# Optimization experiments

Measured on AMD Instinct MI355X. Metric: run time of the kernel, lower is better.

Reference implementation:

```python
import jax, jax.numpy as jnp
import numpy as np

N = 50000
E = 800000
NEG_SLOPE = 0.2


def setup_inputs() -> dict:
    key = jax.random.key(0)
    ks = jax.random.split(key, 12)
    feat = jax.random.normal(ks[0], (N, 256), dtype=jnp.float32)
    src = jax.random.randint(ks[1], (E,), 0, N, dtype=jnp.int32)
    dst = jax.random.randint(ks[2], (E,), 0, N, dtype=jnp.int32)
    # layer 1: in=256 -> H=4, D=64 (concat 256)
    W1 = jax.random.normal(ks[3], (256, 256), dtype=jnp.float32) * (1.0 / np.sqrt(256))
    attn_l1 = jax.random.normal(ks[4], (4, 64), dtype=jnp.float32) * 0.1
    attn_r1 = jax.random.normal(ks[5], (4, 64), dtype=jnp.float32) * 0.1
    bias1 = jnp.zeros((256,), dtype=jnp.float32)
    # layer 2: in=256 -> H=1, D=128
    W2 = jax.random.normal(ks[6], (256, 128), dtype=jnp.float32) * (1.0 / np.sqrt(256))
    attn_l2 = jax.random.normal(ks[7], (1, 128), dtype=jnp.float32) * 0.1
    attn_r2 = jax.random.normal(ks[8], (1, 128), dtype=jnp.float32) * 0.1
    bias2 = jnp.zeros((128,), dtype=jnp.float32)
    return {"feat": feat, "src": src, "dst": dst,
            "W1": W1, "attn_l1": attn_l1, "attn_r1": attn_r1, "bias1": bias1,
            "W2": W2, "attn_l2": attn_l2, "attn_r2": attn_r2, "bias2": bias2}


def gat_conv(feat, src, dst, W, attn_l, attn_r, bias, apply_relu):
    H, D = attn_l.shape
    n = feat.shape[0]
    ft = (feat @ W).reshape(n, H, D)                      # [N,H,D]
    el = jnp.einsum('nhd,hd->nh', ft, attn_l)             # [N,H]
    er = jnp.einsum('nhd,hd->nh', ft, attn_r)             # [N,H]
    e = el[src] + er[dst]                                 # [E,H]  u_add_v
    e = jnp.where(e > 0, e, NEG_SLOPE * e)                # leaky_relu
    # edge softmax grouped by dst
    m = jax.ops.segment_max(e, dst, num_segments=n)       # [N,H]
    ex = jnp.exp(e - m[dst])
    denom = jax.ops.segment_sum(ex, dst, num_segments=n)  # [N,H]
    a = ex / denom[dst]                                   # [E,H]
    msg = ft[src] * a[:, :, None]                         # [E,H,D]
    out = jax.ops.segment_sum(msg, dst, num_segments=n)   # [N,H,D]
    out = out + bias.reshape(1, H, D)
    out = out.reshape(n, H * D)                           # concat_out
    if apply_relu:
        out = jax.nn.relu(out)
    return out


def reference(feat, src, dst, W1, attn_l1, attn_r1, bias1, W2, attn_l2, attn_r2, bias2):
    h = gat_conv(feat, src, dst, W1, attn_l1, attn_r1, bias1, apply_relu=True)
    h = gat_conv(h, src, dst, W2, attn_l2, attn_r2, bias2, apply_relu=False)
    return h
```

## Files before the change

### kernel.cpp

```cpp
#include <hip/hip_runtime.h>

#define NEG_SLOPE 0.2f

typedef short s16x8 __attribute__((ext_vector_type(8)));
typedef float f32x4 __attribute__((ext_vector_type(4)));

__device__ __forceinline__ unsigned short f2bf(float f) {
    unsigned int u = __float_as_uint(f);
    unsigned int r = (u + 0x7fffu + ((u >> 16) & 1u)) >> 16;
    return (unsigned short)r;
}
__device__ __forceinline__ float bf2f(unsigned int us) {
    return __uint_as_float(us << 16);
}


__global__ void fill_k(const int* __restrict__ src, const int* __restrict__ dst,
                       int* __restrict__ cnt, int* __restrict__ ovf_n,
                       int* __restrict__ bucket,
                       int* __restrict__ ovf_dst, int* __restrict__ ovf_src, int E,
                       const float* __restrict__ W1, const float* __restrict__ al1,
                       const float* __restrict__ ar1,
                       const float* __restrict__ W2, const float* __restrict__ al2,
                       const float* __restrict__ ar2,
                       float* __restrict__ wl1, float* __restrict__ wl2,
                       unsigned short* __restrict__ Bt1h, unsigned short* __restrict__ Bt1l,
                       unsigned short* __restrict__ Bt2h, unsigned short* __restrict__ Bt2l) {
    const int b = blockIdx.x;
    if (b == 0) {
        int k = threadIdx.x;
        #pragma unroll
        for (int h = 0; h < 4; h++) {
            float sl = 0.f, sr = 0.f;
            #pragma unroll 8
            for (int d = 0; d < 64; d++) {
                float wv = W1[k * 256 + h * 64 + d];
                sl = fmaf(wv, al1[h * 64 + d], sl);
                sr = fmaf(wv, ar1[h * 64 + d], sr);
            }
            wl1[k * 8 + h] = sl;
            wl1[k * 8 + 4 + h] = sr;
        }
        float sl = 0.f, sr = 0.f;
        #pragma unroll 8
        for (int d = 0; d < 128; d++) {
            float wv = W2[k * 128 + d];
            sl = fmaf(wv, al2[d], sl);
            sr = fmaf(wv, ar2[d], sr);
        }
        wl2[k * 2 + 0] = sl;
        wl2[k * 2 + 1] = sr;
        return;
    }
    if (b <= 4) {
        int c = (b - 1) * 64 + (threadIdx.x >> 2);
        int kq = threadIdx.x & 3;
        #pragma unroll 8
        for (int kk = 0; kk < 64; kk++) {
            int k = kq + kk * 4;
            float w = W1[k * 256 + c];
            unsigned short h = f2bf(w);
            unsigned short l = f2bf(w - bf2f(h));
            Bt1h[c * 256 + k] = h;
            Bt1l[c * 256 + k] = l;
        }
        return;
    }
    if (b <= 6) {
        int c = (b - 5) * 64 + (threadIdx.x >> 2);
        int kq = threadIdx.x & 3;
        #pragma unroll 8
        for (int kk = 0; kk < 64; kk++) {
            int k = kq + kk * 4;
            float w = W2[k * 128 + c];
            unsigned short h = f2bf(w);
            unsigned short l = f2bf(w - bf2f(h));
            Bt2h[c * 256 + k] = h;
            Bt2l[c * 256 + k] = l;
        }
        return;
    }
    int e = (b - 7) * 256 + threadIdx.x;
    if (e < E) {
        int d = dst[e];
        int pos = atomicAdd(&cnt[d], 1);
        if (pos < 64) {
            bucket[(d << 6) + pos] = src[e];
        } else {
            int j = atomicAdd(ovf_n, 1);
            ovf_dst[j] = d;
            ovf_src[j] = src[e];
        }
    }
}


__global__ __launch_bounds__(256) void prep_k(const float* __restrict__ feat,
                                              const float* __restrict__ wl1,
                                              unsigned short* __restrict__ Ah,
                                              unsigned short* __restrict__ Al,
                                              float* __restrict__ el1,
                                              float* __restrict__ er1, int Nn) {
    const int lane = threadIdx.x & 63, wid = threadIdx.x >> 6;
    const int n = blockIdx.x * 4 + wid;
    if (n >= Nn) return;
    float4 f = ((const float4*)(feat + (size_t)n * 256))[lane];
    unsigned short h0 = f2bf(f.x), h1 = f2bf(f.y), h2 = f2bf(f.z), h3 = f2bf(f.w);
    unsigned short l0 = f2bf(f.x - bf2f(h0)), l1 = f2bf(f.y - bf2f(h1));
    unsigned short l2 = f2bf(f.z - bf2f(h2)), l3 = f2bf(f.w - bf2f(h3));
    uint2 hv, lv;
    hv.x = (unsigned)h0 | ((unsigned)h1 << 16);
    hv.y = (unsigned)h2 | ((unsigned)h3 << 16);
    lv.x = (unsigned)l0 | ((unsigned)l1 << 16);
    lv.y = (unsigned)l2 | ((unsigned)l3 << 16);
    ((uint2*)(Ah + (size_t)n * 256))[lane] = hv;
    ((uint2*)(Al + (size_t)n * 256))[lane] = lv;

    float ff[4] = {f.x, f.y, f.z, f.w};
    float pa[4] = {0.f, 0.f, 0.f, 0.f}, pb[4] = {0.f, 0.f, 0.f, 0.f};
    const float* wp = wl1 + lane * 32;
    #pragma unroll
    for (int j = 0; j < 4; j++) {
        float4 wa = *(const float4*)(wp + j * 8);
        float4 wb = *(const float4*)(wp + j * 8 + 4);
        pa[0] = fmaf(ff[j], wa.x, pa[0]); pa[1] = fmaf(ff[j], wa.y, pa[1]);
        pa[2] = fmaf(ff[j], wa.z, pa[2]); pa[3] = fmaf(ff[j], wa.w, pa[3]);
        pb[0] = fmaf(ff[j], wb.x, pb[0]); pb[1] = fmaf(ff[j], wb.y, pb[1]);
        pb[2] = fmaf(ff[j], wb.z, pb[2]); pb[3] = fmaf(ff[j], wb.w, pb[3]);
    }
    #pragma unroll
    for (int h = 0; h < 4; h++) {
        #pragma unroll
        for (int o = 32; o > 0; o >>= 1) {
            pa[h] += __shfl_xor(pa[h], o);
            pb[h] += __shfl_xor(pb[h], o);
        }
    }
    if (lane == 0) {
        ((float4*)el1)[n] = float4{pa[0], pa[1], pa[2], pa[3]};
        ((float4*)er1)[n] = float4{pb[0], pb[1], pb[2], pb[3]};
    }
}


__global__ __launch_bounds__(256) void gemm_k(const unsigned short* __restrict__ Ah,
                                              const unsigned short* __restrict__ Al,
                                              const unsigned short* __restrict__ Bh,
                                              const unsigned short* __restrict__ Bl,
                                              unsigned short* __restrict__ Cb,
                                              int M, int Nc) {
    __shared__ __align__(16) unsigned short As_h[128][56], As_l[128][56];
    __shared__ __align__(16) unsigned short Bs_h[64][56], Bs_l[64][56];

    const int tid = threadIdx.x;
    const int lane = tid & 63, wid = tid >> 6;
    const int row0 = blockIdx.y * 128;
    const int col0 = blockIdx.x * 64;
    const int wm = (wid & 1) * 64;
    const int wn = (wid >> 1) * 32;
    const int quad = lane >> 4, mrow = lane & 15;

    const int a_row = tid >> 1;
    const int a_k = (tid & 1) * 16;
    const int b_col = tid >> 2;
    const int b_k = (tid & 3) * 8;

    const size_t a_off = (size_t)min(row0 + a_row, M - 1) * 256 + a_k;
    const size_t b_off = (size_t)(col0 + b_col) * 256 + b_k;

    f32x4 acc[4][2];
    #pragma unroll
    for (int i = 0; i < 4; i++)
        #pragma unroll
        for (int j = 0; j < 2; j++) acc[i][j] = f32x4{0.f, 0.f, 0.f, 0.f};

    uint4 rah0 = *(const uint4*)(Ah + a_off);
    uint4 rah1 = *(const uint4*)(Ah + a_off + 8);
    uint4 ral0 = *(const uint4*)(Al + a_off);
    uint4 ral1 = *(const uint4*)(Al + a_off + 8);
    uint4 rbh  = *(const uint4*)(Bh + b_off);
    uint4 rbl  = *(const uint4*)(Bl + b_off);

    for (int kt = 0; kt < 8; kt++) {
        __syncthreads();
        *(uint4*)&As_h[a_row][a_k]     = rah0;
        *(uint4*)&As_h[a_row][a_k + 8] = rah1;
        *(uint4*)&As_l[a_row][a_k]     = ral0;
        *(uint4*)&As_l[a_row][a_k + 8] = ral1;
        *(uint4*)&Bs_h[b_col][b_k] = rbh;
        *(uint4*)&Bs_l[b_col][b_k] = rbl;
        __syncthreads();
        if (kt < 7) {
            size_t ao = a_off + (size_t)(kt + 1) * 32;
            size_t bo = b_off + (size_t)(kt + 1) * 32;
            rah0 = *(const uint4*)(Ah + ao);
            rah1 = *(const uint4*)(Ah + ao + 8);
            ral0 = *(const uint4*)(Al + ao);
            ral1 = *(const uint4*)(Al + ao + 8);
            rbh  = *(const uint4*)(Bh + bo);
            rbl  = *(const uint4*)(Bl + bo);
        }
        s16x8 ah[4], al4[4], bh[2], bl[2];
        #pragma unroll
        for (int i = 0; i < 4; i++) {
            ah[i]  = *(const s16x8*)&As_h[wm + 16 * i + mrow][quad * 8];
            al4[i] = *(const s16x8*)&As_l[wm + 16 * i + mrow][quad * 8];
        }
        #pragma unroll
        for (int j = 0; j < 2; j++) {
            bh[j] = *(const s16x8*)&Bs_h[wn + 16 * j + mrow][quad * 8];
            bl[j] = *(const s16x8*)&Bs_l[wn + 16 * j + mrow][quad * 8];
        }
        #pragma unroll
        for (int i = 0; i < 4; i++)
            #pragma unroll
            for (int j = 0; j < 2; j++) {
                acc[i][j] = __builtin_amdgcn_mfma_f32_16x16x32_bf16(ah[i],  bh[j], acc[i][j], 0, 0, 0);
                acc[i][j] = __builtin_amdgcn_mfma_f32_16x16x32_bf16(ah[i],  bl[j], acc[i][j], 0, 0, 0);
                acc[i][j] = __builtin_amdgcn_mfma_f32_16x16x32_bf16(al4[i], bh[j], acc[i][j], 0, 0, 0);
            }
    }

    #pragma unroll
    for (int i = 0; i < 4; i++) {
        #pragma unroll
        for (int j = 0; j < 2; j++) {
            int col = col0 + wn + 16 * j + mrow;
            int rbase = row0 + wm + 16 * i + quad * 4;
            #pragma unroll
            for (int r = 0; r < 4; r++) {
                int row = rbase + r;
                if (row < M) Cb[(size_t)row * Nc + col] = f2bf(acc[i][j][r]);
            }
        }
    }
}


__device__ __forceinline__ void fma8(float* acc, float wgt, uint4 u) {
    acc[0] = fmaf(wgt, bf2f(u.x & 0xffff), acc[0]);
    acc[1] = fmaf(wgt, bf2f(u.x >> 16),    acc[1]);
    acc[2] = fmaf(wgt, bf2f(u.y & 0xffff), acc[2]);
    acc[3] = fmaf(wgt, bf2f(u.y >> 16),    acc[3]);
    acc[4] = fmaf(wgt, bf2f(u.z & 0xffff), acc[4]);
    acc[5] = fmaf(wgt, bf2f(u.z >> 16),    acc[5]);
    acc[6] = fmaf(wgt, bf2f(u.w & 0xffff), acc[6]);
    acc[7] = fmaf(wgt, bf2f(u.w >> 16),    acc[7]);
}

template <int H, int D, bool RELU, bool FUSE2>
__global__ __launch_bounds__(256) void fagg_k(const unsigned short* __restrict__ ft,
                                              const float* __restrict__ el,
                                              const float* __restrict__ er,
                                              const int* __restrict__ cnt,
                                              const int* __restrict__ bucket,
                                              const int* __restrict__ ovf_n,
                                              const int* __restrict__ ovf_dst,
                                              const int* __restrict__ ovf_src,
                                              const float* __restrict__ bias,
                                              float* __restrict__ out, int n_nodes,
                                              unsigned short* __restrict__ oh,
                                              unsigned short* __restrict__ ol,
                                              const float* __restrict__ wl2,
                                              float* __restrict__ el2,
                                              float* __restrict__ er2) {
    constexpr int HD = H * D;
    constexpr int LPE = HD / 8;
    constexpr int EPI = 64 / LPE;
    constexpr int SH = (HD == 256) ? 9 : 8;
    const int lane = threadIdx.x & 63;
    const int w = threadIdx.x >> 6;
    const int n = blockIdx.x * 4 + w;
    __shared__ int   s_src[4][64];
    __shared__ float s_a[4][64 * H];
    if (n >= n_nodes) return;
    const int deg = cnt[n];
    const int lane_sub = lane & (LPE - 1);
    const int q = lane / LPE;
    const int c0 = lane_sub * 8;
    const int h_of = c0 / D;
    const unsigned lsub16 = (unsigned)(lane_sub * 16);
    const char* fb = (const char*)ft;
    const char* eb = (const char*)el;

    float ern[H];
    #pragma unroll
    for (int h = 0; h < H; h++) ern[h] = er[n * H + h];

    float acc[8];
    #pragma unroll
    for (int t = 0; t < 8; t++) acc[t] = 0.f;

    const int* s_src_w = s_src[w];
    const float* s_a_w = s_a[w];

    if (deg <= 64) {
        const bool act = lane < deg;
        int sv = act ? bucket[(n << 6) + lane] : 0;
        s_src[w][lane] = sv;
        float evr[H];
        if constexpr (H == 4) {
            float4 e4 = *(const float4*)(eb + ((unsigned)sv << 4));
            evr[0] = e4.x; evr[1] = e4.y; evr[2] = e4.z; evr[3] = e4.w;
        } else {
            evr[0] = *(const float*)(eb + ((unsigned)sv << 2));
        }
        const int rc = (deg + EPI - 1) & ~(EPI - 1);
        const int nl = rc / EPI;
        const int nl0 = nl < 16 ? nl : 16;
        uint4 vv[8];
        #pragma unroll
        for (int i = 0; i < 8; i++) {
            if (i < nl0) {
                unsigned bo = ((unsigned)s_src_w[i * EPI + q] << SH) + lsub16;
                vv[i] = *(const uint4*)(fb + bo);
            }
        }
        float ex[H], sm[H];
        #pragma unroll
        for (int h = 0; h < H; h++) {
            float t = evr[h] + ern[h];
            t = t > 0.f ? t : NEG_SLOPE * t;
            ex[h] = act ? __expf(t) : 0.f;
            sm[h] = ex[h];
        }
        #pragma unroll
        for (int h = 0; h < H; h++)
            for (int o = 32; o > 0; o >>= 1) sm[h] += __shfl_xor(sm[h], o);
        #pragma unroll
        for (int h = 0; h < H; h++)
            s_a[w][lane * H + h] = ex[h] * (sm[h] > 0.f ? 1.f / sm[h] : 0.f);
        #pragma unroll
        for (int i = 0; i < 16; i++) {
            if (i < nl0) {
                float wt = s_a_w[(i * EPI + q) * H + h_of];
                fma8(acc, wt, vv[i & 7]);
                if (i + 8 < nl0) {
                    unsigned bo = ((unsigned)s_src_w[(i + 8) * EPI + q] << SH) + lsub16;
                    vv[i & 7] = *(const uint4*)(fb + bo);
                }
            }
        }
        for (int e = 16 * EPI + q; e < rc; e += EPI) {
            unsigned bo = ((unsigned)s_src_w[e] << SH) + lsub16;
            uint4 v = *(const uint4*)(fb + bo);
            fma8(acc, s_a_w[e * H + h_of], v);
        }
    } else {
        const int novf = *ovf_n;
        int sv0 = bucket[(n << 6) + lane];
        s_src[w][lane] = sv0;
        float sm[H];
        #pragma unroll
        for (int h = 0; h < H; h++) sm[h] = 0.f;
        {
            float evr[H];
            if constexpr (H == 4) {
                float4 e4 = ((const float4*)el)[sv0];
                evr[0] = e4.x; evr[1] = e4.y; evr[2] = e4.z; evr[3] = e4.w;
            } else evr[0] = el[sv0];
            #pragma unroll
            for (int h = 0; h < H; h++) {
                float t = evr[h] + ern[h];
                t = t > 0.f ? t : NEG_SLOPE * t;
                sm[h] += __expf(t);
            }
        }
        for (int i = lane; i < novf; i += 64) {
            if (ovf_dst[i] == n) {
                int sv = ovf_src[i];
                float evr[H];
                if constexpr (H == 4) {
                    float4 e4 = ((const float4*)el)[sv];
                    evr[0] = e4.x; evr[1] = e4.y; evr[2] = e4.z; evr[3] = e4.w;
                } else evr[0] = el[sv];
                #pragma unroll
                for (int h = 0; h < H; h++) {
                    float t = evr[h] + ern[h];
                    t = t > 0.f ? t : NEG_SLOPE * t;
                    sm[h] += __expf(t);
                }
            }
        }
        #pragma unroll
        for (int h = 0; h < H; h++)
            for (int o = 32; o > 0; o >>= 1) sm[h] += __shfl_xor(sm[h], o);
        float inv[H];
        #pragma unroll
        for (int h = 0; h < H; h++) inv[h] = (sm[h] > 0.f) ? (1.f / sm[h]) : 0.f;
        {
            float evr[H];
            if constexpr (H == 4) {
                float4 e4 = ((const float4*)el)[sv0];
                evr[0] = e4.x; evr[1] = e4.y; evr[2] = e4.z; evr[3] = e4.w;
            } else evr[0] = el[sv0];
            #pragma unroll
            for (int h = 0; h < H; h++) {
                float t = evr[h] + ern[h];
                t = t > 0.f ? t : NEG_SLOPE * t;
                s_a[w][lane * H + h] = __expf(t) * inv[h];
            }
        }
        for (int e = q; e < 64; e += EPI) {
            unsigned bo = ((unsigned)s_src_w[e] << SH) + lsub16;
            uint4 v = *(const uint4*)(fb + bo);
            fma8(acc, s_a_w[e * H + h_of], v);
        }
        for (int i = 0; i < novf; i++) {
            if (ovf_dst[i] != n) continue;
            int sv = ovf_src[i];
            float elh, ernh, invh;
            if constexpr (H == 4) {
                float4 e4 = ((const float4*)el)[sv];
                elh  = (h_of & 2) ? ((h_of & 1) ? e4.w : e4.z)
                                  : ((h_of & 1) ? e4.y : e4.x);
                ernh = (h_of & 2) ? ((h_of & 1) ? ern[3] : ern[2])
                                  : ((h_of & 1) ? ern[1] : ern[0]);
                invh = (h_of & 2) ? ((h_of & 1) ? inv[3] : inv[2])
                                  : ((h_of & 1) ? inv[1] : inv[0]);
            } else {
                elh = el[sv]; ernh = ern[0]; invh = inv[0];
            }
            float t = elh + ernh;
            t = t > 0.f ? t : NEG_SLOPE * t;
            float wt = __expf(t) * invh;
            uint4 v = *(const uint4*)(fb + (((unsigned)sv << SH) + lsub16));
            if (q == 0) fma8(acc, wt, v);
        }
    }

    #pragma unroll
    for (int t = 0; t < 8; t++) {
        #pragma unroll
        for (int s = LPE; s < 64; s <<= 1) acc[t] += __shfl_xor(acc[t], s);
    }
    if (lane < LPE) {
        float4 b0 = ((const float4*)bias)[lane * 2];
        float4 b1 = ((const float4*)bias)[lane * 2 + 1];
        float v[8] = {acc[0] + b0.x, acc[1] + b0.y, acc[2] + b0.z, acc[3] + b0.w,
                      acc[4] + b1.x, acc[5] + b1.y, acc[6] + b1.z, acc[7] + b1.w};
        if (RELU) {
            #pragma unroll
            for (int t = 0; t < 8; t++) v[t] = fmaxf(v[t], 0.f);
        }
        if constexpr (FUSE2) {
            unsigned short hh[8], ll[8];
            #pragma unroll
            for (int t = 0; t < 8; t++) {
                hh[t] = f2bf(v[t]);
                ll[t] = f2bf(v[t] - bf2f(hh[t]));
            }
            uint4 hv, lv;
            hv.x = (unsigned)hh[0] | ((unsigned)hh[1] << 16);
            hv.y = (unsigned)hh[2] | ((unsigned)hh[3] << 16);
            hv.z = (unsigned)hh[4] | ((unsigned)hh[5] << 16);
            hv.w = (unsigned)hh[6] | ((unsigned)hh[7] << 16);
            lv.x = (unsigned)ll[0] | ((unsigned)ll[1] << 16);
            lv.y = (unsigned)ll[2] | ((unsigned)ll[3] << 16);
            lv.z = (unsigned)ll[4] | ((unsigned)ll[5] << 16);
            lv.w = (unsigned)ll[6] | ((unsigned)ll[7] << 16);
            ((uint4*)(oh + (size_t)n * HD))[lane] = hv;
            ((uint4*)(ol + (size_t)n * HD))[lane] = lv;
            float pa = 0.f, pb = 0.f;
            #pragma unroll
            for (int t = 0; t < 8; t++) {
                float2 wv = ((const float2*)wl2)[lane * 8 + t];
                pa = fmaf(v[t], wv.x, pa);
                pb = fmaf(v[t], wv.y, pb);
            }
            #pragma unroll
            for (int o = 16; o > 0; o >>= 1) {
                pa += __shfl_xor(pa, o);
                pb += __shfl_xor(pb, o);
            }
            if (lane == 0) { el2[n] = pa; er2[n] = pb; }
        } else {
            float4 o0{v[0], v[1], v[2], v[3]};
            float4 o1{v[4], v[5], v[6], v[7]};
            float4* op = (float4*)out + (size_t)n * (HD / 4) + lane * 2;
            op[0] = o0;
            op[1] = o1;
        }
    }
}


extern "C" void kernel_launch(void* const* d_in, const int* in_sizes, int n_in,
                              void* d_out, int out_size, void* d_ws, size_t ws_size,
                              hipStream_t stream) {
    const float* feat    = (const float*)d_in[0];
    const int*   src     = (const int*)d_in[1];
    const int*   dst     = (const int*)d_in[2];
    const float* W1      = (const float*)d_in[3];
    const float* attn_l1 = (const float*)d_in[4];
    const float* attn_r1 = (const float*)d_in[5];
    const float* bias1   = (const float*)d_in[6];
    const float* W2      = (const float*)d_in[7];
    const float* attn_l2 = (const float*)d_in[8];
    const float* attn_r2 = (const float*)d_in[9];
    const float* bias2   = (const float*)d_in[10];
    float* out = (float*)d_out;

    const int N = in_sizes[0] / 256;
    const int E = in_sizes[1];
    const int nbE = (E + 255) / 256;

    char* ws = (char*)d_ws;
    size_t o = 0;
    auto alloc = [&](size_t bytes) -> void* {
        void* p = ws + o;
        o = (o + bytes + 255) & ~(size_t)255;
        return p;
    };
    int* cnt     = (int*)alloc((size_t)(N + 64) * 4);
    int* ovf_n   = cnt + N;
    int* bucket  = (int*)alloc((size_t)N * 64 * 4);
    int* ovf_dst = (int*)alloc((size_t)E * 4);
    int* ovf_src = (int*)alloc((size_t)E * 4);
    float* wl1 = (float*)alloc(256 * 8 * 4);
    float* wl2 = (float*)alloc(256 * 2 * 4);
    float* el1 = (float*)alloc((size_t)N * 4 * 4);
    float* er1 = (float*)alloc((size_t)N * 4 * 4);
    float* el2 = (float*)alloc((size_t)N * 4);
    float* er2 = (float*)alloc((size_t)N * 4);
    unsigned short* ft1b = (unsigned short*)alloc((size_t)N * 256 * 2);
    unsigned short* Ah   = (unsigned short*)alloc((size_t)N * 256 * 2);
    unsigned short* Al   = (unsigned short*)alloc((size_t)N * 256 * 2);
    unsigned short* Bt1h = (unsigned short*)alloc((size_t)256 * 256 * 2);
    unsigned short* Bt1l = (unsigned short*)alloc((size_t)256 * 256 * 2);
    unsigned short* Bt2h = (unsigned short*)alloc((size_t)128 * 256 * 2);
    unsigned short* Bt2l = (unsigned short*)alloc((size_t)128 * 256 * 2);
    unsigned short* ft2b = ft1b;
    unsigned short* h1h  = Ah;
    unsigned short* h1l  = Al;

    hipMemsetAsync(cnt, 0, (size_t)(N + 64) * 4, stream);
    fill_k<<<7 + nbE, 256, 0, stream>>>(src, dst, cnt, ovf_n, bucket, ovf_dst, ovf_src, E,
                                        W1, attn_l1, attn_r1, W2, attn_l2, attn_r2,
                                        wl1, wl2, Bt1h, Bt1l, Bt2h, Bt2l);
    prep_k<<<(N + 3) / 4, 256, 0, stream>>>(feat, wl1, Ah, Al, el1, er1, N);

    gemm_k<<<dim3(4, (N + 127) / 128), 256, 0, stream>>>(Ah, Al, Bt1h, Bt1l, ft1b, N, 256);
    fagg_k<4, 64, true, true><<<(N + 3) / 4, 256, 0, stream>>>(ft1b, el1, er1, cnt, bucket,
                                                               ovf_n, ovf_dst, ovf_src,
                                                               bias1, nullptr, N,
                                                               h1h, h1l, wl2, el2, er2);

    gemm_k<<<dim3(2, (N + 127) / 128), 256, 0, stream>>>(h1h, h1l, Bt2h, Bt2l, ft2b, N, 128);
    fagg_k<1, 128, false, false><<<(N + 3) / 4, 256, 0, stream>>>(ft2b, el2, er2, cnt, bucket,
                                                                  ovf_n, ovf_dst, ovf_src,
                                                                  bias2, out, N,
                                                                  nullptr, nullptr, nullptr,
                                                                  nullptr, nullptr);
}
```

Before: 374.5 us.

## Two-pass binned edge partition to replace global atomic bucket fill

Edge bucketing now happens in two passes. First, edges are partitioned into 256-node destination bins using LDS-local counting and one global atomic per bin per block, with (src,dst) pairs written into scratch that reuses the ft1b buffer. Second, one block per bin fills each node's bucket using LDS atomics, merged with the feature prep kernel. This removes the per-edge global atomics on node counters at the cost of an extra pass over the pair data. Correctness now depends on the global overflow count, so any overflow sends every node in aggregation down the slow path.

```diff
diff --git a/kernel.cpp b/kernel.cpp
--- a/kernel.cpp
+++ b/kernel.cpp
@@ -1,6 +1,7 @@
 #include <hip/hip_runtime.h>
 
 #define NEG_SLOPE 0.2f
+#define BIN_CAP 8192
 
 typedef short s16x8 __attribute__((ext_vector_type(8)));
 typedef float f32x4 __attribute__((ext_vector_type(4)));
@@ -15,17 +16,18 @@
 }
 
 
-__global__ void fill_k(const int* __restrict__ src, const int* __restrict__ dst,
-                       int* __restrict__ cnt, int* __restrict__ ovf_n,
-                       int* __restrict__ bucket,
-                       int* __restrict__ ovf_dst, int* __restrict__ ovf_src, int E,
-                       const float* __restrict__ W1, const float* __restrict__ al1,
-                       const float* __restrict__ ar1,
-                       const float* __restrict__ W2, const float* __restrict__ al2,
-                       const float* __restrict__ ar2,
-                       float* __restrict__ wl1, float* __restrict__ wl2,
-                       unsigned short* __restrict__ Bt1h, unsigned short* __restrict__ Bt1l,
-                       unsigned short* __restrict__ Bt2h, unsigned short* __restrict__ Bt2l) {
+__global__ __launch_bounds__(256) void binpart_k(
+        const int* __restrict__ src, const int* __restrict__ dst, int E,
+        int* __restrict__ bin_cur, int* __restrict__ ovf_n,
+        int2* __restrict__ pairs,
+        int* __restrict__ ovf_dst, int* __restrict__ ovf_src,
+        const float* __restrict__ W1, const float* __restrict__ al1,
+        const float* __restrict__ ar1,
+        const float* __restrict__ W2, const float* __restrict__ al2,
+        const float* __restrict__ ar2,
+        float* __restrict__ wl1, float* __restrict__ wl2,
+        unsigned short* __restrict__ Bt1h, unsigned short* __restrict__ Bt1l,
+        unsigned short* __restrict__ Bt2h, unsigned short* __restrict__ Bt2l) {
     const int b = blockIdx.x;
     if (b == 0) {
         int k = threadIdx.x;
@@ -80,29 +82,92 @@
         }
         return;
     }
-    int e = (b - 7) * 256 + threadIdx.x;
-    if (e < E) {
-        int d = dst[e];
-        int pos = atomicAdd(&cnt[d], 1);
-        if (pos < 64) {
-            bucket[(d << 6) + pos] = src[e];
-        } else {
-            int j = atomicAdd(ovf_n, 1);
-            ovf_dst[j] = d;
-            ovf_src[j] = src[e];
-        }
-    }
-}
-
-
-__global__ __launch_bounds__(256) void prep_k(const float* __restrict__ feat,
-                                              const float* __restrict__ wl1,
-                                              unsigned short* __restrict__ Ah,
-                                              unsigned short* __restrict__ Al,
-                                              float* __restrict__ el1,
-                                              float* __restrict__ er1, int Nn) {
+    __shared__ int l_cnt[256];
+    __shared__ int l_base[256];
+    const int tid = threadIdx.x;
+    const int base_e = (b - 7) * 2048 + tid * 8;
+    int s[8], d[8], bn[8], rk[8];
+    bool v[8];
+    if (base_e + 7 < E) {
+        int4 a0 = *(const int4*)(src + base_e);
+        int4 a1 = *(const int4*)(src + base_e + 4);
+        int4 c0 = *(const int4*)(dst + base_e);
+        int4 c1 = *(const int4*)(dst + base_e + 4);
+        s[0]=a0.x; s[1]=a0.y; s[2]=a0.z; s[3]=a0.w;
+        s[4]=a1.x; s[5]=a1.y; s[6]=a1.z; s[7]=a1.w;
+        d[0]=c0.x; d[1]=c0.y; d[2]=c0.z; d[3]=c0.w;
+        d[4]=c1.x; d[5]=c1.y; d[6]=c1.z; d[7]=c1.w;
+        #pragma unroll
+        for (int i = 0; i < 8; i++) v[i] = true;
+    } else {
+        #pragma unroll
+        for (int i = 0; i < 8; i++) {
+            int e = base_e + i;
+            v[i] = e < E;
+            s[i] = v[i] ? src[e] : 0;
+            d[i] = v[i] ? dst[e] : 0;
+        }
+    }
+    l_cnt[tid] = 0;
+    __syncthreads();
+    #pragma unroll
+    for (int i = 0; i < 8; i++) {
+        bn[i] = d[i] >> 8;
+        if (v[i]) rk[i] = atomicAdd(&l_cnt[bn[i]], 1);
+    }
+    __syncthreads();
+    {
+        int c = l_cnt[tid];
+        if (c > 0) l_base[tid] = atomicAdd(&bin_cur[tid * 16], c);
+    }
+    __syncthreads();
+    #pragma unroll
+    for (int i = 0; i < 8; i++) {
+        if (v[i]) {
+            int pos = l_base[bn[i]] + rk[i];
+            if (pos < BIN_CAP) {
+                int2 p; p.x = s[i]; p.y = d[i];
+                pairs[(size_t)bn[i] * BIN_CAP + pos] = p;
+            } else {
+                int j = atomicAdd(ovf_n, 1);
+                ovf_dst[j] = d[i]; ovf_src[j] = s[i];
+            }
+        }
+    }
+}
+
+
+__global__ __launch_bounds__(256) void prepfill_k(
+        const int* __restrict__ bin_cur, const int2* __restrict__ pairs,
+        int* __restrict__ cnt, int* __restrict__ bucket,
+        int* __restrict__ ovf_n, int* __restrict__ ovf_dst, int* __restrict__ ovf_src,
+        const float* __restrict__ feat, const float* __restrict__ wl1,
+        unsigned short* __restrict__ Ah, unsigned short* __restrict__ Al,
+        float* __restrict__ el1, float* __restrict__ er1, int Nn, int nbin) {
+    if ((int)blockIdx.x < nbin) {
+        __shared__ int l_cnt[256];
+        const int b = blockIdx.x;
+        const int tid = threadIdx.x;
+        l_cnt[tid] = 0;
+        __syncthreads();
+        const int ec = min(bin_cur[b * 16], BIN_CAP);
+        const int2* pp = pairs + (size_t)b * BIN_CAP;
+        for (int i = tid; i < ec; i += 256) {
+            int2 p = pp[i];
+            int pos = atomicAdd(&l_cnt[p.y & 255], 1);
+            if (pos < 64) bucket[((size_t)p.y << 6) + pos] = p.x;
+            else {
+                int j = atomicAdd(ovf_n, 1);
+                ovf_dst[j] = p.y; ovf_src[j] = p.x;
+            }
+        }
+        __syncthreads();
+        int node = b * 256 + tid;
+        if (node < Nn) cnt[node] = l_cnt[tid];
+        return;
+    }
     const int lane = threadIdx.x & 63, wid = threadIdx.x >> 6;
-    const int n = blockIdx.x * 4 + wid;
+    const int n = ((int)blockIdx.x - nbin) * 4 + wid;
     if (n >= Nn) return;
     float4 f = ((const float4*)(feat + (size_t)n * 256))[lane];
     unsigned short h0 = f2bf(f.x), h1 = f2bf(f.y), h2 = f2bf(f.z), h3 = f2bf(f.w);
@@ -275,6 +340,7 @@
     __shared__ float s_a[4][64 * H];
     if (n >= n_nodes) return;
     const int deg = cnt[n];
+    const int novf = *ovf_n;
     const int lane_sub = lane & (LPE - 1);
     const int q = lane / LPE;
     const int c0 = lane_sub * 8;
@@ -294,7 +360,7 @@
     const int* s_src_w = s_src[w];
     const float* s_a_w = s_a[w];
 
-    if (deg <= 64) {
+    if (deg <= 64 && novf == 0) {
         const bool act = lane < deg;
         int sv = act ? bucket[(n << 6) + lane] : 0;
         s_src[w][lane] = sv;
@@ -347,8 +413,9 @@
             fma8(acc, s_a_w[e * H + h_of], v);
         }
     } else {
-        const int novf = *ovf_n;
-        int sv0 = bucket[(n << 6) + lane];
+        const int bval = deg < 64 ? deg : 64;
+        const bool act = lane < bval;
+        int sv0 = act ? bucket[(n << 6) + lane] : 0;
         s_src[w][lane] = sv0;
         float sm[H];
         #pragma unroll
@@ -363,7 +430,7 @@
             for (int h = 0; h < H; h++) {
                 float t = evr[h] + ern[h];
                 t = t > 0.f ? t : NEG_SLOPE * t;
-                sm[h] += __expf(t);
+                if (act) sm[h] += __expf(t);
             }
         }
         for (int i = lane; i < novf; i += 64) {
@@ -398,7 +465,7 @@
             for (int h = 0; h < H; h++) {
                 float t = evr[h] + ern[h];
                 t = t > 0.f ? t : NEG_SLOPE * t;
-                s_a[w][lane * H + h] = __expf(t) * inv[h];
+                s_a[w][lane * H + h] = act ? __expf(t) * inv[h] : 0.f;
             }
         }
         for (int e = q; e < 64; e += EPI) {
@@ -503,7 +570,8 @@
 
     const int N = in_sizes[0] / 256;
     const int E = in_sizes[1];
-    const int nbE = (E + 255) / 256;
+    const int nbin = (N + 255) >> 8;
+    const int nbP = (E + 2047) / 2048;
 
     char* ws = (char*)d_ws;
     size_t o = 0;
@@ -512,8 +580,9 @@
         o = (o + bytes + 255) & ~(size_t)255;
         return p;
     };
-    int* cnt     = (int*)alloc((size_t)(N + 64) * 4);
-    int* ovf_n   = cnt + N;
+    int* bin_cur = (int*)alloc(((size_t)nbin * 16 + 64) * 4);
+    int* ovf_n   = bin_cur + (size_t)nbin * 16;
+    int* cnt     = (int*)alloc((size_t)N * 4);
     int* bucket  = (int*)alloc((size_t)N * 64 * 4);
     int* ovf_dst = (int*)alloc((size_t)E * 4);
     int* ovf_src = (int*)alloc((size_t)E * 4);
@@ -533,12 +602,16 @@
     unsigned short* ft2b = ft1b;
     unsigned short* h1h  = Ah;
     unsigned short* h1l  = Al;
-
-    hipMemsetAsync(cnt, 0, (size_t)(N + 64) * 4, stream);
-    fill_k<<<7 + nbE, 256, 0, stream>>>(src, dst, cnt, ovf_n, bucket, ovf_dst, ovf_src, E,
-                                        W1, attn_l1, attn_r1, W2, attn_l2, attn_r2,
-                                        wl1, wl2, Bt1h, Bt1l, Bt2h, Bt2l);
-    prep_k<<<(N + 3) / 4, 256, 0, stream>>>(feat, wl1, Ah, Al, el1, er1, N);
+    int2* pairs = (int2*)ft1b;
+
+    hipMemsetAsync(bin_cur, 0, ((size_t)nbin * 16 + 64) * 4, stream);
+    binpart_k<<<7 + nbP, 256, 0, stream>>>(src, dst, E, bin_cur, ovf_n, pairs,
+                                           ovf_dst, ovf_src,
+                                           W1, attn_l1, attn_r1, W2, attn_l2, attn_r2,
+                                           wl1, wl2, Bt1h, Bt1l, Bt2h, Bt2l);
+    prepfill_k<<<nbin + (N + 3) / 4, 256, 0, stream>>>(bin_cur, pairs, cnt, bucket,
+                                                       ovf_n, ovf_dst, ovf_src,
+                                                       feat, wl1, Ah, Al, el1, er1, N, nbin);
 
     gemm_k<<<dim3(4, (N + 127) / 128), 256, 0, stream>>>(Ah, Al, Bt1h, Bt1l, ft1b, N, 256);
     fagg_k<4, 64, true, true><<<(N + 3) / 4, 256, 0, stream>>>(ft1b, el1, er1, cnt, bucket,
```

Result: faster. 351.0 us (-6.3%).
